# Performance work log

Hardware: AMD Instinct MI355X
Metric: run time of the kernel (lower is better)

## Reference

```python
import jax, jax.numpy as jnp
import numpy as np

N_NODES = 50000
N_EDGES = 800000
D_FEAT = 128


def setup_inputs() -> dict:
    key = jax.random.key(0)
    k1, k2, k3, k4 = jax.random.split(key, 4)
    edge_index = jax.random.randint(k1, (2, N_EDGES), 0, N_NODES, dtype=jnp.int64 if jax.config.jax_enable_x64 else jnp.int32)
    edge_vals = jax.random.uniform(k2, (N_EDGES,), dtype=jnp.float32)
    features = jax.random.normal(k3, (N_NODES, D_FEAT), dtype=jnp.float32)
    bias = jax.random.normal(k4, (D_FEAT,), dtype=jnp.float32)
    return {"edge_index": edge_index, "edge_vals": edge_vals, "features": features, "bias": bias}


def reference(edge_index, edge_vals, features, bias):
    # SpMM: out[dst] += A[dst, src] * X[src], i.e. sparse adjacency @ dense features
    src = edge_index[0]
    dst = edge_index[1]
    msg = features[src] * edge_vals[:, None]          # [E, D] gather + scale
    out = jax.ops.segment_sum(msg, dst, num_segments=features.shape[0])  # [N, D] scatter-add
    return out + bias                                  # fused bias add
```

## Files before the change

### kernel.cpp

```cpp
#include <hip/hip_runtime.h>
#include <hip/hip_bf16.h>

#define D_FEAT 128
#define D4 (D_FEAT / 4)
#define BKT_SHIFT 7
#define BKT_NODES 128
#define NCHUNK 256
#define MAXBKT 512
#define SLOT 5120

__device__ inline unsigned pack_bf2(float lo, float hi) {
    __hip_bfloat162 h = __float22bfloat162_rn(make_float2(lo, hi));
    unsigned u;
    __builtin_memcpy(&u, &h, 4);
    return u;
}

__global__ __launch_bounds__(512) void ka_part_cvt(
        const int* __restrict__ src, const int* __restrict__ dst,
        const float* __restrict__ vals, int E, int chunk, int nbkt,
        int* __restrict__ gcur, int* __restrict__ ovcnt, int4* __restrict__ ov,
        int2* __restrict__ spackA,
        const float4* __restrict__ fin4, uint4* __restrict__ fb4, int n8) {
    int c = blockIdx.x;
    int tid = threadIdx.x;
    if (c < NCHUNK) {
        __shared__ int hist[MAXBKT];
        __shared__ int lcur[MAXBKT];
        for (int i = tid; i < nbkt; i += 512) hist[i] = 0;
        __syncthreads();
        int lo = c * chunk;
        int hi = min(lo + chunk, E);
        for (int i = lo + tid; i < hi; i += 512)
            atomicAdd(&hist[dst[i] >> BKT_SHIFT], 1);
        __syncthreads();
        for (int i = tid; i < nbkt; i += 512) {
            int h = hist[i];
            lcur[i] = h ? (i * SLOT + atomicAdd(&gcur[i], h)) : 0;
        }
        __syncthreads();
        for (int i = lo + tid; i < hi; i += 512) {
            int d = dst[i];
            int s = src[i];
            float v = vals[i];
            int bkt = d >> BKT_SHIFT;
            int pos = atomicAdd(&lcur[bkt], 1);
            if (pos - bkt * SLOT < SLOT) {
                spackA[pos] = make_int2((s & 0xFFFF) |
                                        ((d & (BKT_NODES - 1)) << 16),
                                        __float_as_int(v));
            } else {
                int oi = atomicAdd(ovcnt, 1);
                ov[oi] = make_int4(s, d, __float_as_int(v), 0);
            }
        }
    } else {
        int nb = gridDim.x - NCHUNK;
        int idx = (c - NCHUNK) * 512 + tid;
        int stride = nb * 512;
        for (int i = idx; i < n8; i += stride) {
            float4 a = fin4[2 * i + 0];
            float4 b = fin4[2 * i + 1];
            uint4 o;
            o.x = pack_bf2(a.x, a.y);
            o.y = pack_bf2(a.z, a.w);
            o.z = pack_bf2(b.x, b.y);
            o.w = pack_bf2(b.z, b.w);
            fb4[i] = o;
        }
    }
}

__global__ __launch_bounds__(1024) void kb_sort_gather(
        const int* __restrict__ gcur, const int2* __restrict__ spackA,
        const uint4* __restrict__ feat4u,
        const float4* __restrict__ bias4, float4* __restrict__ out4, int N) {
    __shared__ int hist[BKT_NODES];
    __shared__ int sbuf[BKT_NODES];
    __shared__ int lcur[BKT_NODES];
    __shared__ int2 ls[SLOT];
    int b = blockIdx.x;
    int tid = threadIdx.x;
    int cnt = gcur[b];
    if (cnt > SLOT) cnt = SLOT;
    int base = b * SLOT;

    if (tid < BKT_NODES) hist[tid] = 0;
    __syncthreads();
    for (int i = tid; i < cnt; i += 1024)
        atomicAdd(&hist[(spackA[base + i].x >> 16) & (BKT_NODES - 1)], 1);
    __syncthreads();
    if (tid < 64) {
        int h0 = hist[2 * tid], h1 = hist[2 * tid + 1];
        int s = h0 + h1;
        int v = s;
        for (int off = 1; off < 64; off <<= 1) {
            int t = __shfl_up(v, off, 64);
            if (tid >= off) v += t;
        }
        sbuf[2 * tid]     = v - h1;
        sbuf[2 * tid + 1] = v;
        lcur[2 * tid]     = v - s;
        lcur[2 * tid + 1] = v - h1;
    }
    __syncthreads();
    for (int i = tid; i < cnt; i += 1024) {
        int2 r = spackA[base + i];
        int p = atomicAdd(&lcur[(r.x >> 16) & (BKT_NODES - 1)], 1);
        ls[p] = r;
    }
    __syncthreads();

    int wave = tid >> 6, lane = tid & 63;
    int q  = lane >> 4;
    int ql = lane & 15;
    float4 bvA = bias4[2 * ql];
    float4 bvB = bias4[2 * ql + 1];
    for (int n = wave; n < BKT_NODES; n += 16) {
        int node = (b << BKT_SHIFT) + n;
        if (node >= N) break;
        int lend = sbuf[n];
        int lbeg = lend - hist[n];
        float4 aA = make_float4(0.f, 0.f, 0.f, 0.f);
        float4 aB = make_float4(0.f, 0.f, 0.f, 0.f);
        for (int e0 = lbeg; e0 < lend; e0 += 16) {
            int2 p[4];
            uint4 h[4];
#pragma unroll
            for (int j = 0; j < 4; j++)
                p[j] = ls[min(e0 + 4 * j + q, lend - 1)];
#pragma unroll
            for (int j = 0; j < 4; j++)
                h[j] = feat4u[(size_t)(p[j].x & 0xFFFF) * 16 + ql];
#pragma unroll
            for (int j = 0; j < 4; j++) {
                float v = (e0 + 4 * j + q < lend) ?
                          __int_as_float(p[j].y) : 0.f;
                __hip_bfloat162 b0, b1, b2, b3;
                __builtin_memcpy(&b0, &h[j].x, 4);
                __builtin_memcpy(&b1, &h[j].y, 4);
                __builtin_memcpy(&b2, &h[j].z, 4);
                __builtin_memcpy(&b3, &h[j].w, 4);
                float2 f0 = __bfloat1622float2(b0);
                float2 f1 = __bfloat1622float2(b1);
                float2 f2 = __bfloat1622float2(b2);
                float2 f3 = __bfloat1622float2(b3);
                aA.x += v * f0.x; aA.y += v * f0.y;
                aA.z += v * f1.x; aA.w += v * f1.y;
                aB.x += v * f2.x; aB.y += v * f2.y;
                aB.z += v * f3.x; aB.w += v * f3.y;
            }
        }
#pragma unroll
        for (int m = 16; m <= 32; m <<= 1) {
            aA.x += __shfl_xor(aA.x, m); aA.y += __shfl_xor(aA.y, m);
            aA.z += __shfl_xor(aA.z, m); aA.w += __shfl_xor(aA.w, m);
            aB.x += __shfl_xor(aB.x, m); aB.y += __shfl_xor(aB.y, m);
            aB.z += __shfl_xor(aB.z, m); aB.w += __shfl_xor(aB.w, m);
        }
        if (q == 0) {
            out4[(size_t)node * 32 + 2 * ql] =
                make_float4(aA.x + bvA.x, aA.y + bvA.y,
                            aA.z + bvA.z, aA.w + bvA.w);
            out4[(size_t)node * 32 + 2 * ql + 1] =
                make_float4(aB.x + bvB.x, aB.y + bvB.y,
                            aB.z + bvB.z, aB.w + bvB.w);
        }
    }
}

__global__ __launch_bounds__(256) void k_over(
        const int4* __restrict__ ov, const int* __restrict__ ovcnt,
        const float4* __restrict__ feat4, float* __restrict__ out) {
    int total = *ovcnt;
    long long items = (long long)total * 32;
    long long stride = (long long)gridDim.x * blockDim.x;
    for (long long i = (long long)blockIdx.x * blockDim.x + threadIdx.x;
         i < items; i += stride) {
        int e = (int)(i >> 5);
        int lane = (int)(i & 31);
        int4 r = ov[e];
        float v = __int_as_float(r.z);
        float4 f = feat4[(size_t)r.x * 32 + lane];
        float* o = out + (size_t)r.y * D_FEAT + lane * 4;
        atomicAdd(o + 0, v * f.x);
        atomicAdd(o + 1, v * f.y);
        atomicAdd(o + 2, v * f.z);
        atomicAdd(o + 3, v * f.w);
    }
}


__global__ void init_bias_kernel(float4* __restrict__ out,
                                 const float4* __restrict__ bias, int n4) {
    int i = blockIdx.x * blockDim.x + threadIdx.x;
    if (i < n4) out[i] = bias[i & (D4 - 1)];
}

__global__ void spmm_edge_kernel(const int* __restrict__ src,
                                 const int* __restrict__ dst,
                                 const float* __restrict__ vals,
                                 const float4* __restrict__ feat,
                                 float* __restrict__ out, int n_edges) {
    int tid = blockIdx.x * blockDim.x + threadIdx.x;
    int e = tid >> 5;
    int lane = tid & 31;
    if (e >= n_edges) return;
    int s = src[e];
    int d = dst[e];
    float v = vals[e];
    float4 f = feat[(size_t)s * D4 + lane];
    float* o = out + (size_t)d * D_FEAT + lane * 4;
    atomicAdd(o + 0, v * f.x);
    atomicAdd(o + 1, v * f.y);
    atomicAdd(o + 2, v * f.z);
    atomicAdd(o + 3, v * f.w);
}

extern "C" void kernel_launch(void* const* d_in, const int* in_sizes, int n_in,
                              void* d_out, int out_size, void* d_ws, size_t ws_size,
                              hipStream_t stream) {
    const int* edge_index = (const int*)d_in[0];
    const float* edge_vals = (const float*)d_in[1];
    const float* features  = (const float*)d_in[2];
    const float* bias      = (const float*)d_in[3];

    int E = in_sizes[1];
    int N = in_sizes[2] / D_FEAT;
    const int* src = edge_index;
    const int* dst = edge_index + E;
    float* out = (float*)d_out;

    int nbkt = (N + BKT_NODES - 1) >> BKT_SHIFT;
    int n8 = N * D_FEAT / 8;
    int chunk = (E + NCHUNK - 1) / NCHUNK;

    size_t fb_bytes = (size_t)N * D_FEAT * 2;
    size_t spA_bytes = (size_t)nbkt * SLOT * 8;
    size_t ov_bytes = (size_t)E * 16;
    size_t needed = fb_bytes + spA_bytes + ov_bytes + ((size_t)MAXBKT + 1) * 4;

    bool ok = (ws_size >= needed) && (N >= 1) && (N <= 65536) && (E >= 1) &&
              (in_sizes[3] == D_FEAT) && (nbkt <= MAXBKT);

    if (ok) {
        char* wp = (char*)d_ws;
        uint4* fb16 = (uint4*)wp;                      wp += fb_bytes;
        int2* spackA = (int2*)wp;                      wp += spA_bytes;
        int4* ov     = (int4*)wp;                      wp += ov_bytes;
        int* gcur    = (int*)wp;
        int* ovcnt   = gcur + MAXBKT;

        hipMemsetAsync(gcur, 0, ((size_t)MAXBKT + 1) * 4, stream);

        ka_part_cvt<<<NCHUNK + 256, 512, 0, stream>>>(
            src, dst, edge_vals, E, chunk, nbkt,
            gcur, ovcnt, ov, spackA,
            (const float4*)features, fb16, n8);
        kb_sort_gather<<<nbkt, 1024, 0, stream>>>(
            gcur, spackA, (const uint4*)fb16,
            (const float4*)bias, (float4*)out, N);
        k_over<<<128, 256, 0, stream>>>(ov, ovcnt,
                                        (const float4*)features, out);
    } else {
        int no4 = out_size / 4;
        {
            int block = 256, grid = (no4 + block - 1) / block;
            init_bias_kernel<<<grid, block, 0, stream>>>((float4*)out,
                                                         (const float4*)bias, no4);
        }
        {
            int block = 256;
            long long total = (long long)E * 32;
            int grid = (int)((total + block - 1) / block);
            spmm_edge_kernel<<<grid, block, 0, stream>>>(src, dst, edge_vals,
                                                         (const float4*)features,
                                                         out, E);
        }
    }
}
```

Before: 135.6 us.

## Sort bucket edges by source slab to localize feature gathers across nodes

Buckets shrink from 128 to 64 destination nodes, and the in-block counting sort now keys on (source slab, destination node), with each slab covering 8192 source rows. Each wave processes its four nodes slab by slab, keeping four accumulator pairs live. At any moment all waves then gather features from the same source range, which is meant to improve L2 and cache locality for the random gathers. In exchange it adds a 512-entry block-wide scan with many barriers, more registers (launch bounds now request 4 blocks), and more bucket and overflow bookkeeping.

```diff
diff --git a/kernel.cpp b/kernel.cpp
--- a/kernel.cpp
+++ b/kernel.cpp
@@ -3,11 +3,13 @@
 
 #define D_FEAT 128
 #define D4 (D_FEAT / 4)
-#define BKT_SHIFT 7
-#define BKT_NODES 128
+#define BKT_SHIFT 6
+#define BKT_NODES 64
 #define NCHUNK 256
-#define MAXBKT 512
-#define SLOT 5120
+#define MAXBKT 1024
+#define SLOT 2560
+#define SL_SHIFT 13
+#define SLKEYS 512
 
 __device__ inline unsigned pack_bf2(float lo, float hi) {
     __hip_bfloat162 h = __float22bfloat162_rn(make_float2(lo, hi));
@@ -71,13 +73,13 @@
     }
 }
 
-__global__ __launch_bounds__(1024) void kb_sort_gather(
+__global__ __launch_bounds__(1024, 4) void kb_sort_gather(
         const int* __restrict__ gcur, const int2* __restrict__ spackA,
         const uint4* __restrict__ feat4u,
         const float4* __restrict__ bias4, float4* __restrict__ out4, int N) {
-    __shared__ int hist[BKT_NODES];
-    __shared__ int sbuf[BKT_NODES];
-    __shared__ int lcur[BKT_NODES];
+    __shared__ int hist[SLKEYS];
+    __shared__ int sbuf[SLKEYS];
+    __shared__ int lcur[SLKEYS];
     __shared__ int2 ls[SLOT];
     int b = blockIdx.x;
     int tid = threadIdx.x;
@@ -85,28 +87,30 @@
     if (cnt > SLOT) cnt = SLOT;
     int base = b * SLOT;
 
-    if (tid < BKT_NODES) hist[tid] = 0;
-    __syncthreads();
-    for (int i = tid; i < cnt; i += 1024)
-        atomicAdd(&hist[(spackA[base + i].x >> 16) & (BKT_NODES - 1)], 1);
-    __syncthreads();
-    if (tid < 64) {
-        int h0 = hist[2 * tid], h1 = hist[2 * tid + 1];
-        int s = h0 + h1;
-        int v = s;
-        for (int off = 1; off < 64; off <<= 1) {
-            int t = __shfl_up(v, off, 64);
-            if (tid >= off) v += t;
-        }
-        sbuf[2 * tid]     = v - h1;
-        sbuf[2 * tid + 1] = v;
-        lcur[2 * tid]     = v - s;
-        lcur[2 * tid + 1] = v - h1;
-    }
+    for (int i = tid; i < SLKEYS; i += 1024) hist[i] = 0;
+    __syncthreads();
+    for (int i = tid; i < cnt; i += 1024) {
+        int x = spackA[base + i].x;
+        int key = (((x & 0xFFFF) >> SL_SHIFT) << BKT_SHIFT) |
+                  ((x >> 16) & (BKT_NODES - 1));
+        atomicAdd(&hist[key], 1);
+    }
+    __syncthreads();
+    if (tid < SLKEYS) sbuf[tid] = hist[tid];
+    __syncthreads();
+    for (int off = 1; off < SLKEYS; off <<= 1) {
+        int t = (tid < SLKEYS && tid >= off) ? sbuf[tid - off] : 0;
+        __syncthreads();
+        if (tid < SLKEYS) sbuf[tid] += t;
+        __syncthreads();
+    }
+    if (tid < SLKEYS) lcur[tid] = sbuf[tid] - hist[tid];
     __syncthreads();
     for (int i = tid; i < cnt; i += 1024) {
         int2 r = spackA[base + i];
-        int p = atomicAdd(&lcur[(r.x >> 16) & (BKT_NODES - 1)], 1);
+        int key = (((r.x & 0xFFFF) >> SL_SHIFT) << BKT_SHIFT) |
+                  ((r.x >> 16) & (BKT_NODES - 1));
+        int p = atomicAdd(&lcur[key], 1);
         ls[p] = r;
     }
     __syncthreads();
@@ -114,57 +118,70 @@
     int wave = tid >> 6, lane = tid & 63;
     int q  = lane >> 4;
     int ql = lane & 15;
+    float4 aA[4], aB[4];
+#pragma unroll
+    for (int k = 0; k < 4; k++) {
+        aA[k] = make_float4(0.f, 0.f, 0.f, 0.f);
+        aB[k] = make_float4(0.f, 0.f, 0.f, 0.f);
+    }
+    for (int s = 0; s < 8; ++s) {
+#pragma unroll
+        for (int k = 0; k < 4; ++k) {
+            int n = wave + (k << 4);
+            int key = (s << BKT_SHIFT) + n;
+            int end = sbuf[key];
+            int beg = end - hist[key];
+            for (int e0 = beg; e0 < end; e0 += 16) {
+                int2 p[4];
+                uint4 h[4];
+#pragma unroll
+                for (int j = 0; j < 4; j++) {
+                    int e = e0 + 4 * j + q;
+                    p[j] = ls[e < end ? e : beg];
+                }
+#pragma unroll
+                for (int j = 0; j < 4; j++)
+                    h[j] = feat4u[(size_t)(p[j].x & 0xFFFF) * 16 + ql];
+#pragma unroll
+                for (int j = 0; j < 4; j++) {
+                    float v = (e0 + 4 * j + q < end) ?
+                              __int_as_float(p[j].y) : 0.f;
+                    __hip_bfloat162 b0, b1, b2, b3;
+                    __builtin_memcpy(&b0, &h[j].x, 4);
+                    __builtin_memcpy(&b1, &h[j].y, 4);
+                    __builtin_memcpy(&b2, &h[j].z, 4);
+                    __builtin_memcpy(&b3, &h[j].w, 4);
+                    float2 f0 = __bfloat1622float2(b0);
+                    float2 f1 = __bfloat1622float2(b1);
+                    float2 f2 = __bfloat1622float2(b2);
+                    float2 f3 = __bfloat1622float2(b3);
+                    aA[k].x += v * f0.x; aA[k].y += v * f0.y;
+                    aA[k].z += v * f1.x; aA[k].w += v * f1.y;
+                    aB[k].x += v * f2.x; aB[k].y += v * f2.y;
+                    aB[k].z += v * f3.x; aB[k].w += v * f3.y;
+                }
+            }
+        }
+    }
     float4 bvA = bias4[2 * ql];
     float4 bvB = bias4[2 * ql + 1];
-    for (int n = wave; n < BKT_NODES; n += 16) {
-        int node = (b << BKT_SHIFT) + n;
-        if (node >= N) break;
-        int lend = sbuf[n];
-        int lbeg = lend - hist[n];
-        float4 aA = make_float4(0.f, 0.f, 0.f, 0.f);
-        float4 aB = make_float4(0.f, 0.f, 0.f, 0.f);
-        for (int e0 = lbeg; e0 < lend; e0 += 16) {
-            int2 p[4];
-            uint4 h[4];
-#pragma unroll
-            for (int j = 0; j < 4; j++)
-                p[j] = ls[min(e0 + 4 * j + q, lend - 1)];
-#pragma unroll
-            for (int j = 0; j < 4; j++)
-                h[j] = feat4u[(size_t)(p[j].x & 0xFFFF) * 16 + ql];
-#pragma unroll
-            for (int j = 0; j < 4; j++) {
-                float v = (e0 + 4 * j + q < lend) ?
-                          __int_as_float(p[j].y) : 0.f;
-                __hip_bfloat162 b0, b1, b2, b3;
-                __builtin_memcpy(&b0, &h[j].x, 4);
-                __builtin_memcpy(&b1, &h[j].y, 4);
-                __builtin_memcpy(&b2, &h[j].z, 4);
-                __builtin_memcpy(&b3, &h[j].w, 4);
-                float2 f0 = __bfloat1622float2(b0);
-                float2 f1 = __bfloat1622float2(b1);
-                float2 f2 = __bfloat1622float2(b2);
-                float2 f3 = __bfloat1622float2(b3);
-                aA.x += v * f0.x; aA.y += v * f0.y;
-                aA.z += v * f1.x; aA.w += v * f1.y;
-                aB.x += v * f2.x; aB.y += v * f2.y;
-                aB.z += v * f3.x; aB.w += v * f3.y;
-            }
-        }
+#pragma unroll
+    for (int k = 0; k < 4; ++k) {
+        int node = (b << BKT_SHIFT) + wave + (k << 4);
 #pragma unroll
         for (int m = 16; m <= 32; m <<= 1) {
-            aA.x += __shfl_xor(aA.x, m); aA.y += __shfl_xor(aA.y, m);
-            aA.z += __shfl_xor(aA.z, m); aA.w += __shfl_xor(aA.w, m);
-            aB.x += __shfl_xor(aB.x, m); aB.y += __shfl_xor(aB.y, m);
-            aB.z += __shfl_xor(aB.z, m); aB.w += __shfl_xor(aB.w, m);
-        }
-        if (q == 0) {
+            aA[k].x += __shfl_xor(aA[k].x, m); aA[k].y += __shfl_xor(aA[k].y, m);
+            aA[k].z += __shfl_xor(aA[k].z, m); aA[k].w += __shfl_xor(aA[k].w, m);
+            aB[k].x += __shfl_xor(aB[k].x, m); aB[k].y += __shfl_xor(aB[k].y, m);
+            aB[k].z += __shfl_xor(aB[k].z, m); aB[k].w += __shfl_xor(aB[k].w, m);
+        }
+        if (q == 0 && node < N) {
             out4[(size_t)node * 32 + 2 * ql] =
-                make_float4(aA.x + bvA.x, aA.y + bvA.y,
-                            aA.z + bvA.z, aA.w + bvA.w);
+                make_float4(aA[k].x + bvA.x, aA[k].y + bvA.y,
+                            aA[k].z + bvA.z, aA[k].w + bvA.w);
             out4[(size_t)node * 32 + 2 * ql + 1] =
-                make_float4(aB.x + bvB.x, aB.y + bvB.y,
-                            aB.z + bvB.z, aB.w + bvB.w);
+                make_float4(aB[k].x + bvB.x, aB[k].y + bvB.y,
+                            aB[k].z + bvB.z, aB[k].w + bvB.w);
         }
     }
 }
```

Measured after the change: 190.3 us. 40.4% more time.
